# Kernel optimization log

Hardware: AMD Instinct MI355X
Metric: run time of the kernel (lower is better)

Reference implementation:

```python
import jax, jax.numpy as jnp
import numpy as np

N_TOKENS = 3
EMBED = 10
RNN = 10
N_LABELS = 3
B = 16384
T = 99
EPS = 1e-7  # keras CategoricalCrossentropy clip epsilon


def setup_inputs() -> dict:
    key = jax.random.key(0)
    ks = jax.random.split(key, 8)
    token_ids = jax.random.randint(ks[0], (B, T), 0, N_TOKENS, dtype=jnp.int32)
    label_ids = jax.random.randint(ks[1], (B, T), 0, N_LABELS)
    labels = jax.nn.one_hot(label_ids, N_LABELS, dtype=jnp.float32)
    mask = jnp.ones((B, T), dtype=bool)  # accepted by call() but unused, kept for signature fidelity
    emb_table = jax.random.normal(ks[2], (N_TOKENS, EMBED), jnp.float32) * 0.05
    W = jax.random.normal(ks[3], (EMBED, RNN), jnp.float32) / np.sqrt(EMBED)
    U = jax.random.normal(ks[4], (RNN, RNN), jnp.float32) / np.sqrt(RNN)
    b = jnp.zeros((RNN,), jnp.float32)
    Wo = jax.random.normal(ks[5], (RNN, N_LABELS), jnp.float32) / np.sqrt(RNN)
    bo = jnp.zeros((N_LABELS,), jnp.float32)
    return dict(token_ids=token_ids, labels=labels, mask=mask,
                emb_table=emb_table, W=W, U=U, b=b, Wo=Wo, bo=bo)


def reference(token_ids, labels, mask, emb_table, W, U, b, Wo, bo):
    # Embedding lookup (mask_zero=True -> token 0 is a masked step)
    emb = emb_table[token_ids]                      # [B, T, E]
    step_mask = (token_ids != 0)                    # [B, T]

    def step(h, inp):
        x_t, m_t = inp                              # [B, E], [B]
        h_new = jnp.tanh(x_t @ W + h @ U + b)       # SimpleRNN cell
        # Keras masking: masked timesteps carry previous state/output
        h = jnp.where(m_t[:, None], h_new, h)
        return h, h

    h0 = jnp.zeros((token_ids.shape[0], W.shape[1]), emb.dtype)
    _, states_tb = jax.lax.scan(step, h0, (emb.transpose(1, 0, 2), step_mask.T))
    states = states_tb.transpose(1, 0, 2)           # [B, T, R]

    probs = jax.nn.softmax(states @ Wo + bo, axis=-1)   # Dense(softmax) -> [B, T, L]
    probs_c = jnp.clip(probs, EPS, 1.0)
    loss = jnp.mean(-jnp.sum(labels * jnp.log(probs_c), axis=-1))
    accuracy = jnp.mean((jnp.argmax(probs, axis=-1) == jnp.argmax(labels, axis=-1)).astype(jnp.float32))
    return states, probs, accuracy, loss
```

## Files before the change

kernel.cpp:

```cpp
#include <hip/hip_runtime.h>
#include <math.h>

#define BB 16384
#define TT 99
#define RR 10
#define LL 3

#define QP(v, j) __int_as_float(__builtin_amdgcn_mov_dpp(                     \
    __float_as_int(v), (j) * 0x55, 0xF, 0xF, true))
#define HMIR(v)  __int_as_float(__builtin_amdgcn_mov_dpp(                     \
    __float_as_int(v), 0x141, 0xF, 0xF, true))

template <int TB, int N>
__device__ __forceinline__ void rnn_section(
    uint64_t wq, float& hoA, float& hoB,
    const float (&UA)[RR], const float (&UB)[RR],
    float cA1, float cA2, float cB1, float cB2,
    float* __restrict__ outA, float* __restrict__ outB)
{
#pragma unroll
    for (int u = 0; u < N; ++u) {
        const int sel = (int)(wq & 3);
        wq >>= 2;

        float hg[RR];
        hg[0] = QP(hoA, 0); hg[1] = QP(hoA, 1);
        hg[2] = QP(hoA, 2); hg[3] = QP(hoA, 3);
        const float mr = HMIR(hoA);
        hg[4] = QP(mr, 0);  hg[5] = QP(mr, 1);
        hg[6] = QP(mr, 2);  hg[7] = QP(mr, 3);
        hg[8] = QP(hoB, 0); hg[9] = QP(hoB, 1);

        const bool is1 = (sel == 1);
        float aA0 = is1 ? cA1 : cA2, aB0 = is1 ? cB1 : cB2;
        float aA1 = 0.0f, aB1 = 0.0f;
#pragma unroll
        for (int i = 0; i < 5; ++i) {
            aA0 = fmaf(hg[i],     UA[i],     aA0);
            aA1 = fmaf(hg[5 + i], UA[5 + i], aA1);
            aB0 = fmaf(hg[i],     UB[i],     aB0);
            aB1 = fmaf(hg[5 + i], UB[5 + i], aB1);
        }
        const float eA = __expf(2.0f * (aA0 + aA1));
        const float eB = __expf(2.0f * (aB0 + aB1));
        const float pA = eA + 1.0f, pB = eB + 1.0f;
        const float r  = __builtin_amdgcn_rcpf(pA * pB);
        const float hnA = fmaf(-2.0f * pB, r, 1.0f);
        const float hnB = fmaf(-2.0f * pA, r, 1.0f);
        if (sel != 0) { hoA = hnA; hoB = hnB; }

        outA[(TB + u) * RR] = hoA;
        outB[(TB + u) * RR] = hoB;
    }
}

__global__ __launch_bounds__(256, 2)
void rnn_seq_kernel(const int* __restrict__ tok_ids,
                    const float* __restrict__ emb,
                    const float* __restrict__ W,
                    const float* __restrict__ U,
                    const float* __restrict__ bvec,
                    float* __restrict__ states_out)
{
    __shared__ unsigned char s_tk[4][8 * 100];

    const int tid = threadIdx.x;
    const int w   = tid >> 6;
    const int l   = tid & 63;
    const int r8  = l >> 3;
    const int g   = l & 7;
    const int rowbase = blockIdx.x * 32 + w * 8;

#pragma unroll
    for (int i = 0; i < 13; ++i) {
        const int p = l + 64 * i;
        if (p < 8 * TT) {
            const int r = p / TT;
            s_tk[w][r * 100 + (p - r * TT)] =
                (unsigned char)tok_ids[(size_t)rowbase * TT + p];
        }
    }

    const uint32_t* tp = reinterpret_cast<const uint32_t*>(&s_tk[w][r8 * 100]);
    uint64_t w0 = 0, w1 = 0, w2 = 0, w3 = 0;
#pragma unroll
    for (int t = 0; t < 32; ++t)
        w0 |= (uint64_t)((tp[t >> 2] >> (8 * (t & 3))) & 3) << (2 * t);
#pragma unroll
    for (int t = 32; t < 64; ++t)
        w1 |= (uint64_t)((tp[t >> 2] >> (8 * (t & 3))) & 3) << (2 * (t - 32));
#pragma unroll
    for (int t = 64; t < 96; ++t)
        w2 |= (uint64_t)((tp[t >> 2] >> (8 * (t & 3))) & 3) << (2 * (t - 64));
#pragma unroll
    for (int t = 96; t < 99; ++t)
        w3 |= (uint64_t)((tp[t >> 2] >> (8 * (t & 3))) & 3) << (2 * (t - 96));

    const int qpar = g >> 2;
    int ord[8];
#pragma unroll
    for (int j = 0; j < 4; ++j) {
        ord[j]     = qpar ? 4 + j : j;
        ord[4 + j] = qpar ? 3 - j : 7 - j;
    }
    const int jA = g;
    const int jB = ((g & 3) < 2) ? 8 + (g & 3) : 8;

    float UA[RR], UB[RR];
#pragma unroll
    for (int k2 = 0; k2 < 8; ++k2) {
        UA[k2] = U[ord[k2] * RR + jA];
        UB[k2] = U[ord[k2] * RR + jB];
    }
    UA[8] = U[8 * RR + jA]; UA[9] = U[9 * RR + jA];
    UB[8] = U[8 * RR + jB]; UB[9] = U[9 * RR + jB];

    float cA1 = bvec[jA], cA2 = cA1, cB1 = bvec[jB], cB2 = cB1;
#pragma unroll
    for (int i = 0; i < RR; ++i) {
        const float e1 = emb[RR + i];
        const float e2 = emb[2 * RR + i];
        const float wA = W[i * RR + jA];
        const float wB = W[i * RR + jB];
        cA1 = fmaf(e1, wA, cA1); cA2 = fmaf(e2, wA, cA2);
        cB1 = fmaf(e1, wB, cB1); cB2 = fmaf(e2, wB, cB2);
    }

    float hoA = 0.0f, hoB = 0.0f;
    float* outA = states_out + (size_t)(rowbase + r8) * (TT * RR) + jA;
    float* outB = states_out + (size_t)(rowbase + r8) * (TT * RR) + jB;

    rnn_section< 0, 32>(w0, hoA, hoB, UA, UB, cA1, cA2, cB1, cB2, outA, outB);
    rnn_section<32, 32>(w1, hoA, hoB, UA, UB, cA1, cA2, cB1, cB2, outA, outB);
    rnn_section<64, 32>(w2, hoA, hoB, UA, UB, cA1, cA2, cB1, cB2, outA, outB);
    rnn_section<96,  3>(w3, hoA, hoB, UA, UB, cA1, cA2, cB1, cB2, outA, outB);
}

__global__ __launch_bounds__(256)
void epilogue_kernel(const float* __restrict__ states,
                     const float* __restrict__ labels,
                     const float* __restrict__ Wo,
                     const float* __restrict__ bo,
                     float* __restrict__ probs_out,
                     float* __restrict__ ws)
{
    const int NT     = BB * TT;
    const int tid    = blockIdx.x * 256 + threadIdx.x;
    const int stride = 2048 * 256;

    float Wc0[RR], Wc1[RR], Wc2[RR];
#pragma unroll
    for (int j = 0; j < RR; ++j) {
        Wc0[j] = Wo[j * LL + 0];
        Wc1[j] = Wo[j * LL + 1];
        Wc2[j] = Wo[j * LL + 2];
    }
    const float b0 = bo[0], b1 = bo[1], b2 = bo[2];

    float loss = 0.0f;
    int   corr = 0;

#pragma unroll 1
    for (int idx = tid; idx < NT; idx += stride) {
        const float* hp = states + (size_t)idx * RR;
        float h[RR];
#pragma unroll
        for (int j = 0; j < RR; j += 2) {
            const float2 v = *reinterpret_cast<const float2*>(hp + j);
            h[j] = v.x; h[j + 1] = v.y;
        }
        const float la1 = labels[(size_t)idx * LL + 1];
        const float la2 = labels[(size_t)idx * LL + 2];
        const int   y   = (la1 > 0.5f) ? 1 : ((la2 > 0.5f) ? 2 : 0);

        float l0 = b0, l1 = b1, l2 = b2;
#pragma unroll
        for (int j = 0; j < RR; ++j) {
            l0 = fmaf(h[j], Wc0[j], l0);
            l1 = fmaf(h[j], Wc1[j], l1);
            l2 = fmaf(h[j], Wc2[j], l2);
        }
        const float e0 = __expf(l0), e1 = __expf(l1), e2 = __expf(l2);
        const float S  = e0 + e1 + e2;
        const float rs = __builtin_amdgcn_rcpf(S);
        probs_out[(size_t)idx * LL + 0] = e0 * rs;
        probs_out[(size_t)idx * LL + 1] = e1 * rs;
        probs_out[(size_t)idx * LL + 2] = e2 * rs;

        const float ly = (y == 0) ? l0 : ((y == 1) ? l1 : l2);
        loss += fminf(__logf(S) - ly, 16.11809565f);

        int ap = 0; float pm = l0;
        if (l1 > pm) { ap = 1; pm = l1; }
        if (l2 > pm) { ap = 2; }
        corr += (ap == y) ? 1 : 0;
    }

    __shared__ float sl[4], sc[4];
    float ls = loss, cs = (float)corr;
#pragma unroll
    for (int off = 32; off > 0; off >>= 1) {
        ls += __shfl_down(ls, off, 64);
        cs += __shfl_down(cs, off, 64);
    }
    if ((threadIdx.x & 63) == 0) { sl[threadIdx.x >> 6] = ls; sc[threadIdx.x >> 6] = cs; }
    __syncthreads();
    if (threadIdx.x == 0) {
        ws[blockIdx.x]        = sl[0] + sl[1] + sl[2] + sl[3];
        ws[2048 + blockIdx.x] = sc[0] + sc[1] + sc[2] + sc[3];
    }
}

__global__ __launch_bounds__(256)
void finalize_kernel(const float* __restrict__ ws, float* __restrict__ out_tail)
{
    __shared__ float sl[4], sc[4];
    const int t = threadIdx.x;
    float ls = 0.0f, cs = 0.0f;
#pragma unroll
    for (int i = 0; i < 8; ++i) {
        ls += ws[t + 256 * i];
        cs += ws[2048 + t + 256 * i];
    }
#pragma unroll
    for (int off = 32; off > 0; off >>= 1) {
        ls += __shfl_down(ls, off, 64);
        cs += __shfl_down(cs, off, 64);
    }
    if ((t & 63) == 0) { sl[t >> 6] = ls; sc[t >> 6] = cs; }
    __syncthreads();
    if (t == 0) {
        const float L = sl[0] + sl[1] + sl[2] + sl[3];
        const float C = sc[0] + sc[1] + sc[2] + sc[3];
        const float inv = 1.0f / (float)((size_t)BB * TT);
        out_tail[0] = C * inv;
        out_tail[1] = L * inv;
    }
}

extern "C" void kernel_launch(void* const* d_in, const int* in_sizes, int n_in,
                              void* d_out, int out_size, void* d_ws, size_t ws_size,
                              hipStream_t stream)
{
    const int*   tok    = (const int*)  d_in[0];
    const float* labels = (const float*)d_in[1];
    const float* emb = (const float*)d_in[3];
    const float* W   = (const float*)d_in[4];
    const float* U   = (const float*)d_in[5];
    const float* bv  = (const float*)d_in[6];
    const float* Wo  = (const float*)d_in[7];
    const float* bo  = (const float*)d_in[8];

    float* out    = (float*)d_out;
    float* states = out;
    float* probs  = out + (size_t)BB * TT * RR;
    float* tail   = out + (size_t)BB * TT * (RR + LL);
    float* ws     = (float*)d_ws;

    rnn_seq_kernel<<<512, 256, 0, stream>>>(tok, emb, W, U, bv, states);
    epilogue_kernel<<<2048, 256, 0, stream>>>(states, labels, Wo, bo, probs, ws);
    finalize_kernel<<<1, 256, 0, stream>>>(ws, tail);
}
```

Baseline: 49.49 us.

## Map one hidden unit per lane with 16-lane row groups

Restructures the RNN recurrence so each row is handled by 16 lanes, each owning a single hidden unit, rather than 8 lanes each computing two units. The hidden state is broadcast across the 16 lanes using row-rotate and quad-permute DPP moves, and the U weights are pre-permuted per lane to match that gather order, with zero weights for the 6 padding lanes. This drops the shared reciprocal trick and the second accumulator chain per lane and raises the occupancy hint from 2 to 4 blocks per CU. The cost is twice as many lanes and blocks for the same rows, 6 of every 16 lanes doing wasted work, and a block-wide barrier after loading tokens.

```diff
diff --git a/kernel.cpp b/kernel.cpp
--- a/kernel.cpp
+++ b/kernel.cpp
@@ -8,53 +8,48 @@
 
 #define QP(v, j) __int_as_float(__builtin_amdgcn_mov_dpp(                     \
     __float_as_int(v), (j) * 0x55, 0xF, 0xF, true))
-#define HMIR(v)  __int_as_float(__builtin_amdgcn_mov_dpp(                     \
-    __float_as_int(v), 0x141, 0xF, 0xF, true))
+#define ROR4(v)  __int_as_float(__builtin_amdgcn_mov_dpp(                     \
+    __float_as_int(v), 0x124, 0xF, 0xF, true))
+
+__device__ __forceinline__ void gather16(float v0, float (&hg)[16]) {
+    const float v1 = ROR4(v0);
+    const float v2 = ROR4(v1);
+    const float v3 = ROR4(v2);
+    hg[ 0] = QP(v0, 0); hg[ 1] = QP(v0, 1); hg[ 2] = QP(v0, 2); hg[ 3] = QP(v0, 3);
+    hg[ 4] = QP(v1, 0); hg[ 5] = QP(v1, 1); hg[ 6] = QP(v1, 2); hg[ 7] = QP(v1, 3);
+    hg[ 8] = QP(v2, 0); hg[ 9] = QP(v2, 1); hg[10] = QP(v2, 2); hg[11] = QP(v2, 3);
+    hg[12] = QP(v3, 0); hg[13] = QP(v3, 1); hg[14] = QP(v3, 2); hg[15] = QP(v3, 3);
+}
 
 template <int TB, int N>
 __device__ __forceinline__ void rnn_section(
-    uint64_t wq, float& hoA, float& hoB,
-    const float (&UA)[RR], const float (&UB)[RR],
-    float cA1, float cA2, float cB1, float cB2,
-    float* __restrict__ outA, float* __restrict__ outB)
+    uint64_t wq, float& ho, const float (&UA)[16],
+    float cA1, float cA2, bool owner, float* __restrict__ outp)
 {
 #pragma unroll
     for (int u = 0; u < N; ++u) {
         const int sel = (int)(wq & 3);
         wq >>= 2;
 
-        float hg[RR];
-        hg[0] = QP(hoA, 0); hg[1] = QP(hoA, 1);
-        hg[2] = QP(hoA, 2); hg[3] = QP(hoA, 3);
-        const float mr = HMIR(hoA);
-        hg[4] = QP(mr, 0);  hg[5] = QP(mr, 1);
-        hg[6] = QP(mr, 2);  hg[7] = QP(mr, 3);
-        hg[8] = QP(hoB, 0); hg[9] = QP(hoB, 1);
-
-        const bool is1 = (sel == 1);
-        float aA0 = is1 ? cA1 : cA2, aB0 = is1 ? cB1 : cB2;
-        float aA1 = 0.0f, aB1 = 0.0f;
-#pragma unroll
-        for (int i = 0; i < 5; ++i) {
-            aA0 = fmaf(hg[i],     UA[i],     aA0);
-            aA1 = fmaf(hg[5 + i], UA[5 + i], aA1);
-            aB0 = fmaf(hg[i],     UB[i],     aB0);
-            aB1 = fmaf(hg[5 + i], UB[5 + i], aB1);
-        }
-        const float eA = __expf(2.0f * (aA0 + aA1));
-        const float eB = __expf(2.0f * (aB0 + aB1));
-        const float pA = eA + 1.0f, pB = eB + 1.0f;
-        const float r  = __builtin_amdgcn_rcpf(pA * pB);
-        const float hnA = fmaf(-2.0f * pB, r, 1.0f);
-        const float hnB = fmaf(-2.0f * pA, r, 1.0f);
-        if (sel != 0) { hoA = hnA; hoB = hnB; }
-
-        outA[(TB + u) * RR] = hoA;
-        outB[(TB + u) * RR] = hoB;
-    }
-}
-
-__global__ __launch_bounds__(256, 2)
+        float hg[16];
+        gather16(ho, hg);
+
+        float a0 = (sel == 1) ? cA1 : cA2;
+        float a1 = 0.0f;
+#pragma unroll
+        for (int i = 0; i < 8; ++i) {
+            a0 = fmaf(hg[i],     UA[i],     a0);
+            a1 = fmaf(hg[8 + i], UA[8 + i], a1);
+        }
+        const float e  = __expf(2.0f * (a0 + a1));
+        const float hn = fmaf(-2.0f, __builtin_amdgcn_rcpf(e + 1.0f), 1.0f);
+        if (sel != 0) ho = hn;
+
+        if (owner) outp[(TB + u) * RR] = ho;
+    }
+}
+
+__global__ __launch_bounds__(256, 4)
 void rnn_seq_kernel(const int* __restrict__ tok_ids,
                     const float* __restrict__ emb,
                     const float* __restrict__ W,
@@ -62,26 +57,27 @@
                     const float* __restrict__ bvec,
                     float* __restrict__ states_out)
 {
-    __shared__ unsigned char s_tk[4][8 * 100];
-
-    const int tid = threadIdx.x;
-    const int w   = tid >> 6;
-    const int l   = tid & 63;
-    const int r8  = l >> 3;
-    const int g   = l & 7;
-    const int rowbase = blockIdx.x * 32 + w * 8;
-
-#pragma unroll
-    for (int i = 0; i < 13; ++i) {
-        const int p = l + 64 * i;
-        if (p < 8 * TT) {
+    __shared__ unsigned char s_tk[16 * 100];
+
+    const int tid  = threadIdx.x;
+    const int l    = tid & 63;
+    const int wv   = tid >> 6;
+    const int gl   = l & 15;
+    const int rowl = wv * 4 + (l >> 4);
+    const int row  = blockIdx.x * 16 + rowl;
+
+#pragma unroll
+    for (int i = 0; i < 7; ++i) {
+        const int p = tid + 256 * i;
+        if (p < 16 * TT) {
             const int r = p / TT;
-            s_tk[w][r * 100 + (p - r * TT)] =
-                (unsigned char)tok_ids[(size_t)rowbase * TT + p];
-        }
-    }
-
-    const uint32_t* tp = reinterpret_cast<const uint32_t*>(&s_tk[w][r8 * 100]);
+            s_tk[r * 100 + (p - r * TT)] =
+                (unsigned char)tok_ids[(size_t)blockIdx.x * (16 * TT) + p];
+        }
+    }
+    __syncthreads();
+
+    const uint32_t* tp = reinterpret_cast<const uint32_t*>(&s_tk[rowl * 100]);
     uint64_t w0 = 0, w1 = 0, w2 = 0, w3 = 0;
 #pragma unroll
     for (int t = 0; t < 32; ++t)
@@ -96,44 +92,32 @@
     for (int t = 96; t < 99; ++t)
         w3 |= (uint64_t)((tp[t >> 2] >> (8 * (t & 3))) & 3) << (2 * (t - 96));
 
-    const int qpar = g >> 2;
-    int ord[8];
-#pragma unroll
-    for (int j = 0; j < 4; ++j) {
-        ord[j]     = qpar ? 4 + j : j;
-        ord[4 + j] = qpar ? 3 - j : 7 - j;
-    }
-    const int jA = g;
-    const int jB = ((g & 3) < 2) ? 8 + (g & 3) : 8;
-
-    float UA[RR], UB[RR];
-#pragma unroll
-    for (int k2 = 0; k2 < 8; ++k2) {
-        UA[k2] = U[ord[k2] * RR + jA];
-        UB[k2] = U[ord[k2] * RR + jB];
-    }
-    UA[8] = U[8 * RR + jA]; UA[9] = U[9 * RR + jA];
-    UB[8] = U[8 * RR + jB]; UB[9] = U[9 * RR + jB];
-
-    float cA1 = bvec[jA], cA2 = cA1, cB1 = bvec[jB], cB2 = cB1;
+    float pg[16];
+    gather16((float)gl, pg);
+    const int jA = (gl < 10) ? gl : 9;
+    float UA[16];
+#pragma unroll
+    for (int k = 0; k < 16; ++k) {
+        const int ui = (int)pg[k];
+        UA[k] = (ui < 10) ? U[ui * RR + jA] : 0.0f;
+    }
+
+    float cA1 = bvec[jA], cA2 = cA1;
 #pragma unroll
     for (int i = 0; i < RR; ++i) {
-        const float e1 = emb[RR + i];
-        const float e2 = emb[2 * RR + i];
         const float wA = W[i * RR + jA];
-        const float wB = W[i * RR + jB];
-        cA1 = fmaf(e1, wA, cA1); cA2 = fmaf(e2, wA, cA2);
-        cB1 = fmaf(e1, wB, cB1); cB2 = fmaf(e2, wB, cB2);
-    }
-
-    float hoA = 0.0f, hoB = 0.0f;
-    float* outA = states_out + (size_t)(rowbase + r8) * (TT * RR) + jA;
-    float* outB = states_out + (size_t)(rowbase + r8) * (TT * RR) + jB;
-
-    rnn_section< 0, 32>(w0, hoA, hoB, UA, UB, cA1, cA2, cB1, cB2, outA, outB);
-    rnn_section<32, 32>(w1, hoA, hoB, UA, UB, cA1, cA2, cB1, cB2, outA, outB);
-    rnn_section<64, 32>(w2, hoA, hoB, UA, UB, cA1, cA2, cB1, cB2, outA, outB);
-    rnn_section<96,  3>(w3, hoA, hoB, UA, UB, cA1, cA2, cB1, cB2, outA, outB);
+        cA1 = fmaf(emb[RR + i],     wA, cA1);
+        cA2 = fmaf(emb[2 * RR + i], wA, cA2);
+    }
+
+    const bool owner = (gl < 10);
+    float* outp = states_out + (size_t)row * (TT * RR) + jA;
+    float ho = 0.0f;
+
+    rnn_section< 0, 32>(w0, ho, UA, cA1, cA2, owner, outp);
+    rnn_section<32, 32>(w1, ho, UA, cA1, cA2, owner, outp);
+    rnn_section<64, 32>(w2, ho, UA, cA1, cA2, owner, outp);
+    rnn_section<96,  3>(w3, ho, UA, cA1, cA2, owner, outp);
 }
 
 __global__ __launch_bounds__(256)
@@ -257,7 +241,7 @@
     float* tail   = out + (size_t)BB * TT * (RR + LL);
     float* ws     = (float*)d_ws;
 
-    rnn_seq_kernel<<<512, 256, 0, stream>>>(tok, emb, W, U, bv, states);
+    rnn_seq_kernel<<<BB / 16, 256, 0, stream>>>(tok, emb, W, U, bv, states);
     epilogue_kernel<<<2048, 256, 0, stream>>>(states, labels, Wo, bo, probs, ws);
     finalize_kernel<<<1, 256, 0, stream>>>(ws, tail);
 }
```

Result: slower. 64.66 us (+30.7%).

## Fuse softmax/loss/accuracy epilogue into RNN recurrence kernel

Applied to the files above, without the earlier changes.

Merges the output projection, softmax, cross-entropy and accuracy into the recurrent kernel. Each step computes the previous step's logits from the already-gathered hidden state via DPP lane shuffles, and labels are packed into 2-bit codes alongside tokens in shared memory. This removes the separate epilogue kernel launch and its re-read of the full states tensor from memory. The cost is extra per-step work (exp, rcp, log) on the serial recurrence critical path, plus higher register pressure.

```diff
diff --git a/kernel.cpp b/kernel.cpp
--- a/kernel.cpp
+++ b/kernel.cpp
@@ -11,25 +11,58 @@
 #define HMIR(v)  __int_as_float(__builtin_amdgcn_mov_dpp(                     \
     __float_as_int(v), 0x141, 0xF, 0xF, true))
 
+__device__ __forceinline__ void gather10(float hoA, float hoB, float (&hg)[RR]) {
+    hg[0] = QP(hoA, 0); hg[1] = QP(hoA, 1);
+    hg[2] = QP(hoA, 2); hg[3] = QP(hoA, 3);
+    const float mr = HMIR(hoA);
+    hg[4] = QP(mr, 0);  hg[5] = QP(mr, 1);
+    hg[6] = QP(mr, 2);  hg[7] = QP(mr, 3);
+    hg[8] = QP(hoB, 0); hg[9] = QP(hoB, 1);
+}
+
+__device__ __forceinline__ void epi_step(
+    const float (&hg)[RR], int yv, int tep, int g,
+    const float (&Wc)[RR], float boc,
+    float* __restrict__ prow, float& loss, int& corr)
+{
+    float lg = boc;
+#pragma unroll
+    for (int i = 0; i < RR; ++i) lg = fmaf(hg[i], Wc[i], lg);
+    const float eo = __expf(lg);
+    const float e0 = QP(eo, 0), e1 = QP(eo, 1), e2 = QP(eo, 2);
+    const float S  = e0 + e1 + e2;
+    const float rs = __builtin_amdgcn_rcpf(S);
+    if (g < 3) prow[tep * LL + g] = eo * rs;
+
+    const float ey = (yv == 0) ? e0 : ((yv == 1) ? e1 : e2);
+    const float py = fmaxf(ey * rs, 1e-7f);
+    const float lt = -__logf(py);
+
+    int ap = 0; float pm = e0;
+    if (e1 > pm) { ap = 1; pm = e1; }
+    if (e2 > pm) { ap = 2; }
+    if (g == 0) { loss += lt; corr += (ap == yv) ? 1 : 0; }
+}
+
 template <int TB, int N>
 __device__ __forceinline__ void rnn_section(
-    uint64_t wq, float& hoA, float& hoB,
+    uint64_t wsel, uint64_t wy, float& hoA, float& hoB,
     const float (&UA)[RR], const float (&UB)[RR],
+    const float (&Wc)[RR], float boc,
     float cA1, float cA2, float cB1, float cB2,
-    float* __restrict__ outA, float* __restrict__ outB)
+    float* __restrict__ outA, float* __restrict__ outB,
+    float* __restrict__ prow, int g, float& loss, int& corr)
 {
 #pragma unroll
     for (int u = 0; u < N; ++u) {
-        const int sel = (int)(wq & 3);
-        wq >>= 2;
+        const int sel = (int)(wsel & 3); wsel >>= 2;
+        const int yv  = (int)(wy & 3);   wy >>= 2;
 
         float hg[RR];
-        hg[0] = QP(hoA, 0); hg[1] = QP(hoA, 1);
-        hg[2] = QP(hoA, 2); hg[3] = QP(hoA, 3);
-        const float mr = HMIR(hoA);
-        hg[4] = QP(mr, 0);  hg[5] = QP(mr, 1);
-        hg[6] = QP(mr, 2);  hg[7] = QP(mr, 3);
-        hg[8] = QP(hoB, 0); hg[9] = QP(hoB, 1);
+        gather10(hoA, hoB, hg);
+
+        if (TB + u > 0)
+            epi_step(hg, yv, TB + u - 1, g, Wc, boc, prow, loss, corr);
 
         const bool is1 = (sel == 1);
         float aA0 = is1 ? cA1 : cA2, aB0 = is1 ? cB1 : cB2;
@@ -55,14 +88,19 @@
 }
 
 __global__ __launch_bounds__(256, 2)
-void rnn_seq_kernel(const int* __restrict__ tok_ids,
-                    const float* __restrict__ emb,
-                    const float* __restrict__ W,
-                    const float* __restrict__ U,
-                    const float* __restrict__ bvec,
-                    float* __restrict__ states_out)
-{
-    __shared__ unsigned char s_tk[4][8 * 100];
+void rnn_fused_kernel(const int* __restrict__ tok_ids,
+                      const float* __restrict__ labels,
+                      const float* __restrict__ emb,
+                      const float* __restrict__ W,
+                      const float* __restrict__ U,
+                      const float* __restrict__ bvec,
+                      const float* __restrict__ Wo,
+                      const float* __restrict__ bo,
+                      float* __restrict__ states_out,
+                      float* __restrict__ probs_out,
+                      float* __restrict__ ws)
+{
+    __shared__ unsigned char s_code[4][8 * 100];
 
     const int tid = threadIdx.x;
     const int w   = tid >> 6;
@@ -75,26 +113,34 @@
     for (int i = 0; i < 13; ++i) {
         const int p = l + 64 * i;
         if (p < 8 * TT) {
-            const int r = p / TT;
-            s_tk[w][r * 100 + (p - r * TT)] =
-                (unsigned char)tok_ids[(size_t)rowbase * TT + p];
+            const size_t gi = (size_t)rowbase * TT + p;
+            const int   tk  = tok_ids[gi];
+            const float la1 = labels[gi * LL + 1];
+            const float la2 = labels[gi * LL + 2];
+            const int   y   = (la1 > 0.5f) ? 1 : ((la2 > 0.5f) ? 2 : 0);
+            const int   r   = p / TT;
+            s_code[w][r * 100 + (p - r * TT)] = (unsigned char)((tk << 2) | y);
         }
     }
 
-    const uint32_t* tp = reinterpret_cast<const uint32_t*>(&s_tk[w][r8 * 100]);
-    uint64_t w0 = 0, w1 = 0, w2 = 0, w3 = 0;
-#pragma unroll
-    for (int t = 0; t < 32; ++t)
-        w0 |= (uint64_t)((tp[t >> 2] >> (8 * (t & 3))) & 3) << (2 * t);
-#pragma unroll
-    for (int t = 32; t < 64; ++t)
-        w1 |= (uint64_t)((tp[t >> 2] >> (8 * (t & 3))) & 3) << (2 * (t - 32));
-#pragma unroll
-    for (int t = 64; t < 96; ++t)
-        w2 |= (uint64_t)((tp[t >> 2] >> (8 * (t & 3))) & 3) << (2 * (t - 64));
-#pragma unroll
-    for (int t = 96; t < 99; ++t)
-        w3 |= (uint64_t)((tp[t >> 2] >> (8 * (t & 3))) & 3) << (2 * (t - 96));
+    const unsigned char* cp = &s_code[w][r8 * 100];
+    uint64_t sw0 = 0, sw1 = 0, sw2 = 0, sw3 = 0;
+    uint64_t yw0 = 0, yw1 = 0, yw2 = 0, yw3 = 0;
+#pragma unroll
+    for (int t = 0; t < TT; ++t) {
+        const uint64_t c  = (uint64_t)cp[t];
+        const uint64_t sv = (c >> 2) & 3, yv = c & 3;
+        if (t < 32)              sw0 |= sv << (2 * t);
+        else if (t < 64)         sw1 |= sv << (2 * (t - 32));
+        else if (t < 96)         sw2 |= sv << (2 * (t - 64));
+        else                     sw3 |= sv << (2 * (t - 96));
+        const int s2 = t + 1;
+        if (s2 < 32)             yw0 |= yv << (2 * s2);
+        else if (s2 < 64)        yw1 |= yv << (2 * (s2 - 32));
+        else if (s2 < 96)        yw2 |= yv << (2 * (s2 - 64));
+        else                     yw3 |= yv << (2 * (s2 - 96));
+    }
+    const int y98 = (int)((yw3 >> 6) & 3);
 
     const int qpar = g >> 2;
     int ord[8];
@@ -105,15 +151,19 @@
     }
     const int jA = g;
     const int jB = ((g & 3) < 2) ? 8 + (g & 3) : 8;
-
-    float UA[RR], UB[RR];
+    const int gc = ((g & 3) < 2) ? (g & 3) : 2;
+
+    float UA[RR], UB[RR], Wc[RR];
 #pragma unroll
     for (int k2 = 0; k2 < 8; ++k2) {
         UA[k2] = U[ord[k2] * RR + jA];
         UB[k2] = U[ord[k2] * RR + jB];
+        Wc[k2] = Wo[ord[k2] * LL + gc];
     }
     UA[8] = U[8 * RR + jA]; UA[9] = U[9 * RR + jA];
     UB[8] = U[8 * RR + jB]; UB[9] = U[9 * RR + jB];
+    Wc[8] = Wo[8 * LL + gc]; Wc[9] = Wo[9 * LL + gc];
+    const float boc = bo[gc];
 
     float cA1 = bvec[jA], cA2 = cA1, cB1 = bvec[jB], cB2 = cB1;
 #pragma unroll
@@ -126,88 +176,40 @@
         cB1 = fmaf(e1, wB, cB1); cB2 = fmaf(e2, wB, cB2);
     }
 
+    const int row = rowbase + r8;
+    float* outA = states_out + (size_t)row * (TT * RR) + jA;
+    float* outB = states_out + (size_t)row * (TT * RR) + jB;
+    float* prow = probs_out  + (size_t)row * (TT * LL);
+
     float hoA = 0.0f, hoB = 0.0f;
-    float* outA = states_out + (size_t)(rowbase + r8) * (TT * RR) + jA;
-    float* outB = states_out + (size_t)(rowbase + r8) * (TT * RR) + jB;
-
-    rnn_section< 0, 32>(w0, hoA, hoB, UA, UB, cA1, cA2, cB1, cB2, outA, outB);
-    rnn_section<32, 32>(w1, hoA, hoB, UA, UB, cA1, cA2, cB1, cB2, outA, outB);
-    rnn_section<64, 32>(w2, hoA, hoB, UA, UB, cA1, cA2, cB1, cB2, outA, outB);
-    rnn_section<96,  3>(w3, hoA, hoB, UA, UB, cA1, cA2, cB1, cB2, outA, outB);
-}
-
-__global__ __launch_bounds__(256)
-void epilogue_kernel(const float* __restrict__ states,
-                     const float* __restrict__ labels,
-                     const float* __restrict__ Wo,
-                     const float* __restrict__ bo,
-                     float* __restrict__ probs_out,
-                     float* __restrict__ ws)
-{
-    const int NT     = BB * TT;
-    const int tid    = blockIdx.x * 256 + threadIdx.x;
-    const int stride = 2048 * 256;
-
-    float Wc0[RR], Wc1[RR], Wc2[RR];
-#pragma unroll
-    for (int j = 0; j < RR; ++j) {
-        Wc0[j] = Wo[j * LL + 0];
-        Wc1[j] = Wo[j * LL + 1];
-        Wc2[j] = Wo[j * LL + 2];
-    }
-    const float b0 = bo[0], b1 = bo[1], b2 = bo[2];
-
     float loss = 0.0f;
     int   corr = 0;
 
-#pragma unroll 1
-    for (int idx = tid; idx < NT; idx += stride) {
-        const float* hp = states + (size_t)idx * RR;
-        float h[RR];
-#pragma unroll
-        for (int j = 0; j < RR; j += 2) {
-            const float2 v = *reinterpret_cast<const float2*>(hp + j);
-            h[j] = v.x; h[j + 1] = v.y;
-        }
-        const float la1 = labels[(size_t)idx * LL + 1];
-        const float la2 = labels[(size_t)idx * LL + 2];
-        const int   y   = (la1 > 0.5f) ? 1 : ((la2 > 0.5f) ? 2 : 0);
-
-        float l0 = b0, l1 = b1, l2 = b2;
-#pragma unroll
-        for (int j = 0; j < RR; ++j) {
-            l0 = fmaf(h[j], Wc0[j], l0);
-            l1 = fmaf(h[j], Wc1[j], l1);
-            l2 = fmaf(h[j], Wc2[j], l2);
-        }
-        const float e0 = __expf(l0), e1 = __expf(l1), e2 = __expf(l2);
-        const float S  = e0 + e1 + e2;
-        const float rs = __builtin_amdgcn_rcpf(S);
-        probs_out[(size_t)idx * LL + 0] = e0 * rs;
-        probs_out[(size_t)idx * LL + 1] = e1 * rs;
-        probs_out[(size_t)idx * LL + 2] = e2 * rs;
-
-        const float ly = (y == 0) ? l0 : ((y == 1) ? l1 : l2);
-        loss += fminf(__logf(S) - ly, 16.11809565f);
-
-        int ap = 0; float pm = l0;
-        if (l1 > pm) { ap = 1; pm = l1; }
-        if (l2 > pm) { ap = 2; }
-        corr += (ap == y) ? 1 : 0;
-    }
-
-    __shared__ float sl[4], sc[4];
+    rnn_section< 0, 32>(sw0, yw0, hoA, hoB, UA, UB, Wc, boc,
+                        cA1, cA2, cB1, cB2, outA, outB, prow, g, loss, corr);
+    rnn_section<32, 32>(sw1, yw1, hoA, hoB, UA, UB, Wc, boc,
+                        cA1, cA2, cB1, cB2, outA, outB, prow, g, loss, corr);
+    rnn_section<64, 32>(sw2, yw2, hoA, hoB, UA, UB, Wc, boc,
+                        cA1, cA2, cB1, cB2, outA, outB, prow, g, loss, corr);
+    rnn_section<96,  3>(sw3, yw3, hoA, hoB, UA, UB, Wc, boc,
+                        cA1, cA2, cB1, cB2, outA, outB, prow, g, loss, corr);
+
+    {
+        float hg[RR];
+        gather10(hoA, hoB, hg);
+        epi_step(hg, y98, 98, g, Wc, boc, prow, loss, corr);
+    }
+
     float ls = loss, cs = (float)corr;
 #pragma unroll
     for (int off = 32; off > 0; off >>= 1) {
         ls += __shfl_down(ls, off, 64);
         cs += __shfl_down(cs, off, 64);
     }
-    if ((threadIdx.x & 63) == 0) { sl[threadIdx.x >> 6] = ls; sc[threadIdx.x >> 6] = cs; }
-    __syncthreads();
-    if (threadIdx.x == 0) {
-        ws[blockIdx.x]        = sl[0] + sl[1] + sl[2] + sl[3];
-        ws[2048 + blockIdx.x] = sc[0] + sc[1] + sc[2] + sc[3];
+    if (l == 0) {
+        const int wid = blockIdx.x * 4 + w;
+        ws[wid]        = ls;
+        ws[2048 + wid] = cs;
     }
 }
 
@@ -257,7 +259,7 @@
     float* tail   = out + (size_t)BB * TT * (RR + LL);
     float* ws     = (float*)d_ws;
 
-    rnn_seq_kernel<<<512, 256, 0, stream>>>(tok, emb, W, U, bv, states);
-    epilogue_kernel<<<2048, 256, 0, stream>>>(states, labels, Wo, bo, probs, ws);
+    rnn_fused_kernel<<<BB / 32, 256, 0, stream>>>(tok, labels, emb, W, U, bv,
+                                                  Wo, bo, states, probs, ws);
     finalize_kernel<<<1, 256, 0, stream>>>(ws, tail);
 }
```

New measurement: 57.44 us. 1.16x slower.
